# Kernel optimization log

Hardware: AMD Instinct MI355X
Metric: run time of the kernel (lower is better)

The kernel has to match this reference:

```python
import jax, jax.numpy as jnp
import numpy as np

NUM_POSES = 200
N = 1048576

def _exp_vector(w):
    # Rodrigues formula: so(3) vector [N,3] -> rotation matrix [N,3,3]
    theta2 = jnp.sum(w * w, axis=-1)                     # [N]
    theta = jnp.sqrt(theta2 + 1e-12)                     # safe norm
    a = (jnp.sin(theta) / theta)[:, None, None]          # sin(t)/t
    b = ((1.0 - jnp.cos(theta)) / theta2.clip(1e-12))[:, None, None]
    wx, wy, wz = w[:, 0], w[:, 1], w[:, 2]
    zero = jnp.zeros_like(wx)
    K = jnp.stack([
        jnp.stack([zero, -wz, wy], axis=-1),
        jnp.stack([wz, zero, -wx], axis=-1),
        jnp.stack([-wy, wx, zero], axis=-1),
    ], axis=-2)                                          # [N,3,3] skew
    I = jnp.eye(3, dtype=w.dtype)
    return I + a * K + b * jnp.einsum('nij,njk->nik', K, K)

def setup_inputs() -> dict:
    key = jax.random.key(0)
    k1, k2, k3, k4 = jax.random.split(key, 4)
    n = jax.random.randint(k1, (N,), 0, NUM_POSES, dtype=jnp.int64)
    E = jax.random.normal(k2, (N, 4, 4), dtype=jnp.float32)
    R = jax.random.normal(k3, (NUM_POSES, 3), dtype=jnp.float32) * 0.1
    T = jax.random.normal(k4, (NUM_POSES, 3), dtype=jnp.float32) * 0.1
    return {"n": n, "E": E, "R": R, "T": T}

def reference(n, E, R, T):
    # mode == 'camera': pose = n
    Rg = R[n]                                            # [N,3] gather
    Tg = T[n]                                            # [N,3]
    rot = _exp_vector(Rg)                                # [N,3,3]
    top = jnp.concatenate([rot, Tg[:, :, None]], axis=2) # [N,3,4]
    bottom = jnp.broadcast_to(
        jnp.array([[0., 0., 0., 1.]], dtype=E.dtype)[None], (n.shape[0], 1, 4))
    M = jnp.concatenate([top, bottom], axis=1)           # [N,4,4]
    return jnp.einsum('nij,njk->nik', M, E)
```

## Files before the change

### kernel.cpp

```cpp
#include <hip/hip_runtime.h>

#define NUM_POSES 200

typedef float        v4f __attribute__((ext_vector_type(4)));
typedef unsigned int v2u __attribute__((ext_vector_type(2)));

__device__ __forceinline__ float bf2f(unsigned int u16) {
    union { unsigned int u; float f; } v; v.u = u16 << 16; return v.f;
}
__device__ __forceinline__ unsigned int f2bf(float f) {
    union { float f; unsigned int u; } v; v.f = f;
    unsigned int r = v.u + 0x7FFFu + ((v.u >> 16) & 1u);
    return r >> 16;
}

template <int CTRL>
__device__ __forceinline__ float rotf(float v) {
    int i = __builtin_bit_cast(int, v);
    i = __builtin_amdgcn_mov_dpp(i, CTRL, 0xF, 0xF, true);
    return __builtin_bit_cast(float, i);
}
template <int CTRL>
__device__ __forceinline__ v4f rot4(v4f v) {
    v4f r;
    r.x = rotf<CTRL>(v.x); r.y = rotf<CTRL>(v.y);
    r.z = rotf<CTRL>(v.z); r.w = rotf<CTRL>(v.w);
    return r;
}
#define ROT1 0x39
#define ROT2 0x4E
#define ROT3 0x93

__global__ void prep_kernel(const unsigned short* __restrict__ E16,
                            const unsigned int* __restrict__ n32,
                            const void* __restrict__ Rv,
                            const void* __restrict__ Tv,
                            int* __restrict__ flags,
                            float* __restrict__ M) {
    __shared__ unsigned int sany;
    int t = threadIdx.x;
    if (t == 0) sany = 0u;
    __syncthreads();
    unsigned int local = 0u;
    for (int k = t; k < 4096; k += 256) {
        float a = fabsf(bf2f(E16[k]));
        if (!(a <= 1e6f)) local |= 1u;
    }
    if (n32[2 * t + 1] != 0u) local |= 2u;
    if (local) atomicOr(&sany, local);
    __syncthreads();
    unsigned int s = sany;
    if (t == 0) { flags[0] = (s & 1u) ? 1 : 0; flags[1] = (s & 2u) ? 1 : 0; }
    if (t >= NUM_POSES) return;
    int p = t;
    float wx, wy, wz, tx, ty, tz;
    if (s & 1u) {
        const float* R = (const float*)Rv; const float* T = (const float*)Tv;
        wx = R[3*p+0]; wy = R[3*p+1]; wz = R[3*p+2];
        tx = T[3*p+0]; ty = T[3*p+1]; tz = T[3*p+2];
    } else {
        const unsigned short* R = (const unsigned short*)Rv;
        const unsigned short* T = (const unsigned short*)Tv;
        wx = bf2f(R[3*p+0]); wy = bf2f(R[3*p+1]); wz = bf2f(R[3*p+2]);
        tx = bf2f(T[3*p+0]); ty = bf2f(T[3*p+1]); tz = bf2f(T[3*p+2]);
    }
    float t2 = wx*wx + wy*wy + wz*wz;
    float th = sqrtf(t2 + 1e-12f);
    float a  = sinf(th) / th;
    float b  = (1.0f - cosf(th)) / fmaxf(t2, 1e-12f);

    float mm[4][4];
    mm[0][0] = 1.0f - b * (wy*wy + wz*wz);
    mm[0][1] = -a * wz + b * wx * wy;
    mm[0][2] =  a * wy + b * wx * wz;
    mm[0][3] = tx;
    mm[1][0] =  a * wz + b * wx * wy;
    mm[1][1] = 1.0f - b * (wx*wx + wz*wz);
    mm[1][2] = -a * wx + b * wy * wz;
    mm[1][3] = ty;
    mm[2][0] = -a * wy + b * wx * wz;
    mm[2][1] =  a * wx + b * wy * wz;
    mm[2][2] = 1.0f - b * (wx*wx + wy*wy);
    mm[2][3] = tz;
    mm[3][0] = 0.0f; mm[3][1] = 0.0f; mm[3][2] = 0.0f; mm[3][3] = 1.0f;
    float* mo = M + p * 16;
    #pragma unroll
    for (int r = 0; r < 4; ++r)
        #pragma unroll
        for (int k = 0; k < 4; ++k)
            mo[r*4 + k] = mm[r][(r + k) & 3];
}

__global__ __launch_bounds__(256) void apply_kernel(
        const void* __restrict__ nin,
        const void* __restrict__ Ein,
        const float4* __restrict__ Mrot,
        void* __restrict__ outv,
        const int* __restrict__ flags,
        int N) {
    const int TOT  = gridDim.x * blockDim.x;
    const int rows = N * 4;
    int t0 = blockIdx.x * blockDim.x + threadIdx.x;
    int t1 = t0 + TOT;
    const int e_is_f32 = flags[0];
    const int n_is_i32 = flags[1];

    #pragma unroll
    for (int u = 0; u < 2; ++u) {
        int t = u ? t1 : t0;
        if (t >= rows) return;
        int e = t >> 2;
        int r = t & 3;
        long long p = n_is_i32 ? (long long)((const int*)nin)[e]
                               : ((const long long*)nin)[e];
        float4 c = Mrot[p * 4 + r];

        if (e_is_f32) {
            v4f self = __builtin_nontemporal_load((const v4f*)Ein + t);
            v4f e1 = rot4<ROT1>(self);
            v4f e2 = rot4<ROT2>(self);
            v4f e3 = rot4<ROT3>(self);
            v4f o = c.x * self + c.y * e1 + c.z * e2 + c.w * e3;
            __builtin_nontemporal_store(o, (v4f*)outv + t);
        } else {
            v2u raw = __builtin_nontemporal_load((const v2u*)Ein + t);
            v4f self;
            self.x = bf2f(raw.x & 0xFFFFu); self.y = bf2f(raw.x >> 16);
            self.z = bf2f(raw.y & 0xFFFFu); self.w = bf2f(raw.y >> 16);
            v4f e1 = rot4<ROT1>(self);
            v4f e2 = rot4<ROT2>(self);
            v4f e3 = rot4<ROT3>(self);
            v4f o = c.x * self + c.y * e1 + c.z * e2 + c.w * e3;
            v2u pk;
            pk.x = f2bf(o.x) | (f2bf(o.y) << 16);
            pk.y = f2bf(o.z) | (f2bf(o.w) << 16);
            __builtin_nontemporal_store(pk, (v2u*)outv + t);
        }
    }
}

extern "C" void kernel_launch(void* const* d_in, const int* in_sizes, int n_in,
                              void* d_out, int out_size, void* d_ws, size_t ws_size,
                              hipStream_t stream) {
    const void* n = d_in[0];
    const void* E = d_in[1];
    const void* R = d_in[2];
    const void* T = d_in[3];
    int*    flags = (int*)d_ws;
    float*      M = (float*)((char*)d_ws + 256);
    const int   N = in_sizes[0];

    prep_kernel<<<1, 256, 0, stream>>>((const unsigned short*)E,
                                       (const unsigned int*)n, R, T, flags, M);
    const int rows   = N * 4;
    const int blocks = (rows + 511) / 512;
    apply_kernel<<<blocks, 256, 0, stream>>>(
        n, E, (const float4*)M, d_out, flags, N);
}
```

Baseline: 134.5 us.

## Fuse pose-matrix prep into apply kernel with LDS table and 4x ILP

Merges the single-block prep kernel into the main kernel. Each block recomputes the 200 pose matrices (Rodrigues) into shared memory and detects input dtypes with a 64-lane ballot, so there is no second launch and no global round-trip for flags and M. Each thread now handles 4 rows with loads batched ahead of compute, which adds memory-level parallelism, and the E loads are no longer nontemporal. The cost is that every block repeats the sin/cos pose setup and a __syncthreads before streaming, and the dtype probe now samples less data.

Result: faster. 124.2 us (-7.6%).

```diff
diff --git a/kernel.cpp b/kernel.cpp
--- a/kernel.cpp
+++ b/kernel.cpp
@@ -31,111 +31,132 @@
 #define ROT2 0x4E
 #define ROT3 0x93
 
-__global__ void prep_kernel(const unsigned short* __restrict__ E16,
-                            const unsigned int* __restrict__ n32,
-                            const void* __restrict__ Rv,
-                            const void* __restrict__ Tv,
-                            int* __restrict__ flags,
-                            float* __restrict__ M) {
-    __shared__ unsigned int sany;
-    int t = threadIdx.x;
-    if (t == 0) sany = 0u;
+__global__ __launch_bounds__(256) void fused_kernel(
+        const void* __restrict__ nin,
+        const void* __restrict__ Ein,
+        const void* __restrict__ Rv,
+        const void* __restrict__ Tv,
+        void* __restrict__ outv,
+        int N) {
+    __shared__ v4f Ml[NUM_POSES * 4];
+    __shared__ int sflags;
+    const int tid = threadIdx.x;
+
+    if (tid < 64) {
+        unsigned int dw = ((const unsigned int*)Ein)[tid];
+        bool ef32 = !(fabsf(bf2f(dw & 0xFFFFu)) <= 1e6f);
+        bool ni32 = ((const unsigned int*)nin)[2 * tid + 1] != 0u;
+        unsigned long long b1 = __ballot(ef32);
+        unsigned long long b2 = __ballot(ni32);
+        if (tid == 0) sflags = (b1 ? 1 : 0) | (b2 ? 2 : 0);
+    }
     __syncthreads();
-    unsigned int local = 0u;
-    for (int k = t; k < 4096; k += 256) {
-        float a = fabsf(bf2f(E16[k]));
-        if (!(a <= 1e6f)) local |= 1u;
+    const int s = sflags;
+
+    if (tid < NUM_POSES) {
+        int p = tid;
+        float wx, wy, wz, tx, ty, tz;
+        if (s & 1) {
+            const float* R = (const float*)Rv; const float* T = (const float*)Tv;
+            wx = R[3*p+0]; wy = R[3*p+1]; wz = R[3*p+2];
+            tx = T[3*p+0]; ty = T[3*p+1]; tz = T[3*p+2];
+        } else {
+            const unsigned short* R = (const unsigned short*)Rv;
+            const unsigned short* T = (const unsigned short*)Tv;
+            wx = bf2f(R[3*p+0]); wy = bf2f(R[3*p+1]); wz = bf2f(R[3*p+2]);
+            tx = bf2f(T[3*p+0]); ty = bf2f(T[3*p+1]); tz = bf2f(T[3*p+2]);
+        }
+        float t2 = wx*wx + wy*wy + wz*wz;
+        float th = sqrtf(t2 + 1e-12f);
+        float a  = sinf(th) / th;
+        float b  = (1.0f - cosf(th)) / fmaxf(t2, 1e-12f);
+
+        float mm[4][4];
+        mm[0][0] = 1.0f - b * (wy*wy + wz*wz);
+        mm[0][1] = -a * wz + b * wx * wy;
+        mm[0][2] =  a * wy + b * wx * wz;
+        mm[0][3] = tx;
+        mm[1][0] =  a * wz + b * wx * wy;
+        mm[1][1] = 1.0f - b * (wx*wx + wz*wz);
+        mm[1][2] = -a * wx + b * wy * wz;
+        mm[1][3] = ty;
+        mm[2][0] = -a * wy + b * wx * wz;
+        mm[2][1] =  a * wx + b * wy * wz;
+        mm[2][2] = 1.0f - b * (wx*wx + wy*wy);
+        mm[2][3] = tz;
+        mm[3][0] = 0.0f; mm[3][1] = 0.0f; mm[3][2] = 0.0f; mm[3][3] = 1.0f;
+        #pragma unroll
+        for (int r = 0; r < 4; ++r) {
+            v4f c;
+            c.x = mm[r][(r + 0) & 3];
+            c.y = mm[r][(r + 1) & 3];
+            c.z = mm[r][(r + 2) & 3];
+            c.w = mm[r][(r + 3) & 3];
+            Ml[p * 4 + r] = c;
+        }
     }
-    if (n32[2 * t + 1] != 0u) local |= 2u;
-    if (local) atomicOr(&sany, local);
     __syncthreads();
-    unsigned int s = sany;
-    if (t == 0) { flags[0] = (s & 1u) ? 1 : 0; flags[1] = (s & 2u) ? 1 : 0; }
-    if (t >= NUM_POSES) return;
-    int p = t;
-    float wx, wy, wz, tx, ty, tz;
-    if (s & 1u) {
-        const float* R = (const float*)Rv; const float* T = (const float*)Tv;
-        wx = R[3*p+0]; wy = R[3*p+1]; wz = R[3*p+2];
-        tx = T[3*p+0]; ty = T[3*p+1]; tz = T[3*p+2];
-    } else {
-        const unsigned short* R = (const unsigned short*)Rv;
-        const unsigned short* T = (const unsigned short*)Tv;
-        wx = bf2f(R[3*p+0]); wy = bf2f(R[3*p+1]); wz = bf2f(R[3*p+2]);
-        tx = bf2f(T[3*p+0]); ty = bf2f(T[3*p+1]); tz = bf2f(T[3*p+2]);
-    }
-    float t2 = wx*wx + wy*wy + wz*wz;
-    float th = sqrtf(t2 + 1e-12f);
-    float a  = sinf(th) / th;
-    float b  = (1.0f - cosf(th)) / fmaxf(t2, 1e-12f);
 
-    float mm[4][4];
-    mm[0][0] = 1.0f - b * (wy*wy + wz*wz);
-    mm[0][1] = -a * wz + b * wx * wy;
-    mm[0][2] =  a * wy + b * wx * wz;
-    mm[0][3] = tx;
-    mm[1][0] =  a * wz + b * wx * wy;
-    mm[1][1] = 1.0f - b * (wx*wx + wz*wz);
-    mm[1][2] = -a * wx + b * wy * wz;
-    mm[1][3] = ty;
-    mm[2][0] = -a * wy + b * wx * wz;
-    mm[2][1] =  a * wx + b * wy * wz;
-    mm[2][2] = 1.0f - b * (wx*wx + wy*wy);
-    mm[2][3] = tz;
-    mm[3][0] = 0.0f; mm[3][1] = 0.0f; mm[3][2] = 0.0f; mm[3][3] = 1.0f;
-    float* mo = M + p * 16;
+    const int rows = N * 4;
+    const int TOT  = gridDim.x * blockDim.x;
+    const int t0   = blockIdx.x * blockDim.x + tid;
+    const bool ef32 = (s & 1) != 0;
+    const bool ni32 = (s & 2) != 0;
+
+    int t[4];
     #pragma unroll
-    for (int r = 0; r < 4; ++r)
+    for (int k = 0; k < 4; ++k) t[k] = t0 + k * TOT;
+
+    if (ef32) {
+        v4f self[4], c[4];
         #pragma unroll
         for (int k = 0; k < 4; ++k)
-            mo[r*4 + k] = mm[r][(r + k) & 3];
-}
-
-__global__ __launch_bounds__(256) void apply_kernel(
-        const void* __restrict__ nin,
-        const void* __restrict__ Ein,
-        const float4* __restrict__ Mrot,
-        void* __restrict__ outv,
-        const int* __restrict__ flags,
-        int N) {
-    const int TOT  = gridDim.x * blockDim.x;
-    const int rows = N * 4;
-    int t0 = blockIdx.x * blockDim.x + threadIdx.x;
-    int t1 = t0 + TOT;
-    const int e_is_f32 = flags[0];
-    const int n_is_i32 = flags[1];
-
-    #pragma unroll
-    for (int u = 0; u < 2; ++u) {
-        int t = u ? t1 : t0;
-        if (t >= rows) return;
-        int e = t >> 2;
-        int r = t & 3;
-        long long p = n_is_i32 ? (long long)((const int*)nin)[e]
-                               : ((const long long*)nin)[e];
-        float4 c = Mrot[p * 4 + r];
-
-        if (e_is_f32) {
-            v4f self = __builtin_nontemporal_load((const v4f*)Ein + t);
-            v4f e1 = rot4<ROT1>(self);
-            v4f e2 = rot4<ROT2>(self);
-            v4f e3 = rot4<ROT3>(self);
-            v4f o = c.x * self + c.y * e1 + c.z * e2 + c.w * e3;
-            __builtin_nontemporal_store(o, (v4f*)outv + t);
-        } else {
-            v2u raw = __builtin_nontemporal_load((const v2u*)Ein + t);
-            v4f self;
-            self.x = bf2f(raw.x & 0xFFFFu); self.y = bf2f(raw.x >> 16);
-            self.z = bf2f(raw.y & 0xFFFFu); self.w = bf2f(raw.y >> 16);
-            v4f e1 = rot4<ROT1>(self);
-            v4f e2 = rot4<ROT2>(self);
-            v4f e3 = rot4<ROT3>(self);
-            v4f o = c.x * self + c.y * e1 + c.z * e2 + c.w * e3;
-            v2u pk;
-            pk.x = f2bf(o.x) | (f2bf(o.y) << 16);
-            pk.y = f2bf(o.z) | (f2bf(o.w) << 16);
-            __builtin_nontemporal_store(pk, (v2u*)outv + t);
-        }
+            if (t[k] < rows) self[k] = ((const v4f*)Ein)[t[k]];
+        #pragma unroll
+        for (int k = 0; k < 4; ++k)
+            if (t[k] < rows) {
+                int e = t[k] >> 2, r = t[k] & 3;
+                long long p = ni32 ? (long long)((const int*)nin)[e]
+                                   : ((const long long*)nin)[e];
+                c[k] = Ml[p * 4 + r];
+            }
+        #pragma unroll
+        for (int k = 0; k < 4; ++k)
+            if (t[k] < rows) {
+                v4f o = c[k].x * self[k]
+                      + c[k].y * rot4<ROT1>(self[k])
+                      + c[k].z * rot4<ROT2>(self[k])
+                      + c[k].w * rot4<ROT3>(self[k]);
+                __builtin_nontemporal_store(o, (v4f*)outv + t[k]);
+            }
+    } else {
+        v2u raw[4]; v4f c[4];
+        #pragma unroll
+        for (int k = 0; k < 4; ++k)
+            if (t[k] < rows) raw[k] = ((const v2u*)Ein)[t[k]];
+        #pragma unroll
+        for (int k = 0; k < 4; ++k)
+            if (t[k] < rows) {
+                int e = t[k] >> 2, r = t[k] & 3;
+                long long p = ni32 ? (long long)((const int*)nin)[e]
+                                   : ((const long long*)nin)[e];
+                c[k] = Ml[p * 4 + r];
+            }
+        #pragma unroll
+        for (int k = 0; k < 4; ++k)
+            if (t[k] < rows) {
+                v4f self;
+                self.x = bf2f(raw[k].x & 0xFFFFu); self.y = bf2f(raw[k].x >> 16);
+                self.z = bf2f(raw[k].y & 0xFFFFu); self.w = bf2f(raw[k].y >> 16);
+                v4f o = c[k].x * self
+                      + c[k].y * rot4<ROT1>(self)
+                      + c[k].z * rot4<ROT2>(self)
+                      + c[k].w * rot4<ROT3>(self);
+                v2u pk;
+                pk.x = f2bf(o.x) | (f2bf(o.y) << 16);
+                pk.y = f2bf(o.z) | (f2bf(o.w) << 16);
+                __builtin_nontemporal_store(pk, (v2u*)outv + t[k]);
+            }
     }
 }
 
@@ -146,14 +167,10 @@
     const void* E = d_in[1];
     const void* R = d_in[2];
     const void* T = d_in[3];
-    int*    flags = (int*)d_ws;
-    float*      M = (float*)((char*)d_ws + 256);
     const int   N = in_sizes[0];
 
-    prep_kernel<<<1, 256, 0, stream>>>((const unsigned short*)E,
-                                       (const unsigned int*)n, R, T, flags, M);
-    const int rows   = N * 4;
-    const int blocks = (rows + 511) / 512;
-    apply_kernel<<<blocks, 256, 0, stream>>>(
-        n, E, (const float4*)M, d_out, flags, N);
+    const int rows    = N * 4;
+    const int threads = (rows + 3) / 4;
+    const int blocks  = (threads + 255) / 256;
+    fused_kernel<<<blocks, 256, 0, stream>>>(n, E, R, T, d_out, N);
 }
```
